# Optimization experiments

Hardware: AMD Instinct MI355X
Metric: run time of the kernel (lower is better)

Reference implementation:

```python
import jax, jax.numpy as jnp
import numpy as np
from jax import lax

N_KERNELS = 11
N_GRAMS = 3
EMB = 300
CONV_OUT = 128
B, QLEN, DLEN = 128, 30, 256


def _kernel_mus(n):
    mus = [1.0]
    bin_size = 2.0 / (n - 1)
    mus.append(1 - bin_size / 2)
    for i in range(1, n - 1):
        mus.append(mus[i] - bin_size)
    return mus


def _kernel_sigmas(n):
    bin_size = 2.0 / (n - 1)
    return [0.001] + [0.5 * bin_size] * (n - 1)


MU = jnp.asarray(np.array(_kernel_mus(N_KERNELS), dtype=np.float32))      # [K]
SIGMA = jnp.asarray(np.array(_kernel_sigmas(N_KERNELS), dtype=np.float32))  # [K]


def setup_inputs() -> dict:
    key = jax.random.key(0)
    ks = jax.random.split(key, 10)
    inp = {
        "query_embeddings": jax.random.normal(ks[0], (B, QLEN, EMB), jnp.float32),
        "document_embeddings": jax.random.normal(ks[1], (B, DLEN, EMB), jnp.float32),
        "query_pad_oov_mask": jnp.ones((B, QLEN), jnp.float32),
        "document_pad_oov_mask": jnp.ones((B, DLEN), jnp.float32),
    }
    # conv weights for n-gram sizes 1..3: [out_ch, in_ch, ksize]
    for i in range(1, N_GRAMS + 1):
        inp[f"conv_w{i}"] = jax.random.normal(ks[1 + i], (CONV_OUT, EMB, i), jnp.float32) * 0.05
        inp[f"conv_b{i}"] = jnp.zeros((CONV_OUT,), jnp.float32)
    inp["dense_w"] = jax.random.uniform(ks[9], (1, N_KERNELS * N_GRAMS * N_GRAMS), jnp.float32,
                                        minval=-0.014, maxval=0.014)
    return inp


def _conv_ngram(x, w, b):
    # x: [B, L, E]; w: [C, E, k]; right-pad by k-1 so output length == L (ConstantPad1d((0,k-1)))
    k = w.shape[-1]
    y = lax.conv_general_dilated(x.transpose(0, 2, 1), w, (1,), [(0, k - 1)],
                                 dimension_numbers=("NCH", "OIH", "NCH"))
    return jax.nn.relu(y + b[None, :, None]).transpose(0, 2, 1)  # [B, L, C]


def _kernel_pool(q, d, qd_mask, q_mask):
    # cosine matrix (AllenNLP CosineMatrixAttention: normalize with +1e-13 eps)
    qn = q / (jnp.linalg.norm(q, axis=-1, keepdims=True) + 1e-13)
    dn = d / (jnp.linalg.norm(d, axis=-1, keepdims=True) + 1e-13)
    cos = jnp.einsum("bqe,bde->bqd", qn, dn) * qd_mask  # [B, Q, D]
    # RBF soft-histogram kernels: [B, Q, D, K]
    k = jnp.exp(-(cos[..., None] - MU) ** 2 / (2.0 * SIGMA ** 2)) * qd_mask[..., None]
    per_kernel_query = k.sum(axis=2)  # [B, Q, K]
    log_pk = jnp.log(jnp.clip(per_kernel_query, 1e-10, None)) * 0.01
    return (log_pk * q_mask[..., None]).sum(axis=1)  # [B, K]


def reference(query_embeddings, document_embeddings, query_pad_oov_mask, document_pad_oov_mask,
              conv_w1, conv_b1, conv_w2, conv_b2, conv_w3, conv_b3, dense_w):
    qd_mask = query_pad_oov_mask[:, :, None] * document_pad_oov_mask[:, None, :]  # [B, Q, D]
    conv_params = [(conv_w1, conv_b1), (conv_w2, conv_b2), (conv_w3, conv_b3)]
    q_res = [_conv_ngram(query_embeddings, w, b) for w, b in conv_params]
    d_res = [_conv_ngram(document_embeddings, w, b) for w, b in conv_params]
    matched = [_kernel_pool(q_res[i], d_res[t], qd_mask, query_pad_oov_mask)
               for i in range(N_GRAMS) for t in range(N_GRAMS)]
    all_grams = jnp.concatenate(matched, axis=1)  # [B, K*9]
    return jnp.squeeze(all_grams @ dense_w.T, axis=1)  # [B]
```

## Files before the change

kernel.cpp:

```cpp
#include <hip/hip_runtime.h>
#include <math.h>


typedef __bf16 bf16x8 __attribute__((ext_vector_type(8)));
typedef float f32x4 __attribute__((ext_vector_type(4)));

#if __has_builtin(__builtin_amdgcn_exp2f)
#define EXP2F(x) __builtin_amdgcn_exp2f(x)
#else
#define EXP2F(x) exp2f(x)
#endif

#define AS_STRIDE 344

static __device__ __forceinline__ unsigned short f2bf(float f) {
  union { float f; unsigned int u; } v; v.f = f;
  unsigned int r = v.u + 0x7FFFu + ((v.u >> 16) & 1u);
  return (unsigned short)(r >> 16);
}

__global__ __launch_bounds__(256) void prep_w(
    const float* __restrict__ w1, const float* __restrict__ w2,
    const float* __restrict__ w3, unsigned short* __restrict__ wt2) {
  int idx = blockIdx.x * 256 + threadIdx.x;
  if (idx >= 245760) return;
  int jj   = idx & 7;
  int lane = (idx >> 3) & 63;
  int ec   = (idx >> 9) % 10;
  int cb   = (idx / 5120) & 7;
  int p    = idx / 40960;
  const float* w; int k, jt;
  if (p == 0)      { w = w1; k = 1; jt = 0; }
  else if (p <= 2) { w = w2; k = 2; jt = p - 1; }
  else             { w = w3; k = 3; jt = p - 3; }
  int c = cb * 16 + (lane & 15);
  int e = ec * 32 + (lane >> 4) * 8 + jj;
  float v = (e < 300) ? w[(c * 300 + e) * k + jt] : 0.0f;
  wt2[idx] = f2bf(v);
}

template<int NI>
__device__ __forceinline__ void conv_body(
    unsigned short* As, float* psq,
    const float* __restrict__ xs, int L, int l0, int b,
    const unsigned short* __restrict__ wt2,
    const float* __restrict__ b1, const float* __restrict__ b2,
    const float* __restrict__ b3,
    unsigned short* __restrict__ out) {
  constexpr int ROWS = NI * 16 + 2;
  constexpr int NR = NI * 16;
  const int t = threadIdx.x;
  const int w = __builtin_amdgcn_readfirstlane(t >> 6);
  const int lane = t & 63;
  const int quad = lane >> 4, lrow = lane & 15;

  for (int idx = t; idx < ROWS * 40; idx += 512) {
    int r = idx / 40, c = idx % 40;
    int l = l0 + r;
    int e = c * 8;
    float4 a = make_float4(0.f, 0.f, 0.f, 0.f);
    float4 cc = make_float4(0.f, 0.f, 0.f, 0.f);
    if (l < L) {
      const float* src = xs + (size_t)l * 300;
      if (e < 300)     a  = *reinterpret_cast<const float4*>(src + e);
      if (e + 4 < 300) cc = *reinterpret_cast<const float4*>(src + e + 4);
    }
    uint4 o;
    o.x = (unsigned int)f2bf(a.x) | ((unsigned int)f2bf(a.y) << 16);
    o.y = (unsigned int)f2bf(a.z) | ((unsigned int)f2bf(a.w) << 16);
    o.z = (unsigned int)f2bf(cc.x) | ((unsigned int)f2bf(cc.y) << 16);
    o.w = (unsigned int)f2bf(cc.z) | ((unsigned int)f2bf(cc.w) << 16);
    *reinterpret_cast<uint4*>(&As[r * AS_STRIDE + c * 8]) = o;
  }

  f32x4 acc[NI][3];
  #pragma unroll
  for (int ni = 0; ni < NI; ++ni)
    #pragma unroll
    for (int g = 0; g < 3; ++g) acc[ni][g] = (f32x4){0.f, 0.f, 0.f, 0.f};

  const unsigned short* wl = wt2 + (size_t)lane * 8;

  auto wfld = [&](bf16x8* dst, int ec) {
    #pragma unroll
    for (int p = 0; p < 6; ++p)
      dst[p] = *reinterpret_cast<const bf16x8*>(
          wl + ((((p * 8 + w) * 10 + ec) << 9)));
  };

  auto compute = [&](const bf16x8* wf, int ec) {
    bf16x8 xf[3][NI];
    #pragma unroll
    for (int j = 0; j < 3; ++j)
      #pragma unroll
      for (int ni = 0; ni < NI; ++ni)
        xf[j][ni] = *reinterpret_cast<const bf16x8*>(
            &As[(ni * 16 + lrow + j) * AS_STRIDE + ec * 32 + quad * 8]);
    const int PJ[6] = {0, 0, 1, 0, 1, 2};
    const int PG[6] = {0, 1, 1, 2, 2, 2};
    #pragma unroll
    for (int p = 0; p < 6; ++p)
      #pragma unroll
      for (int ni = 0; ni < NI; ++ni)
        acc[ni][PG[p]] = __builtin_amdgcn_mfma_f32_16x16x32_bf16(
            wf[p], xf[PJ[p]][ni], acc[ni][PG[p]], 0, 0, 0);
  };

  bf16x8 wfA[6], wfB[6];
  wfld(wfA, 0);
  __syncthreads();

  #pragma unroll
  for (int ec = 0; ec < 10; ec += 2) {
    wfld(wfB, ec + 1);
    compute(wfA, ec);
    if (ec + 2 < 10) wfld(wfA, ec + 2);
    compute(wfB, ec + 1);
  }

  const float* biases[3] = {b1, b2, b3};
  float4 bv[3];
  #pragma unroll
  for (int g = 0; g < 3; ++g)
    bv[g] = *reinterpret_cast<const float4*>(biases[g] + w * 16 + quad * 4);

  #pragma unroll
  for (int ni = 0; ni < NI; ++ni) {
    #pragma unroll
    for (int g = 0; g < 3; ++g) {
      float p = 0.f;
      #pragma unroll
      for (int r = 0; r < 4; ++r) {
        float y = fmaxf(acc[ni][g][r] + bv[g][r], 0.f);
        p += y * y;
      }
      p += __shfl_xor(p, 16);
      p += __shfl_xor(p, 32);
      if (lane < 16) psq[(w * 3 + g) * NR + ni * 16 + lrow] = p;
    }
  }
  __syncthreads();

  #pragma unroll
  for (int ni = 0; ni < NI; ++ni) {
    int row = ni * 16 + lrow;
    int l = l0 + row;
    if (l < L) {
      #pragma unroll
      for (int g = 0; g < 3; ++g) {
        float ssq = 0.f;
        #pragma unroll
        for (int wv = 0; wv < 8; ++wv) ssq += psq[(wv * 3 + g) * NR + row];
        float inv = 1.0f / (sqrtf(ssq) + 1e-13f);
        unsigned int pk[2];
        #pragma unroll
        for (int h = 0; h < 2; ++h) {
          float y0 = fmaxf(acc[ni][g][2 * h + 0] + bv[g][2 * h + 0], 0.f) * inv;
          float y1 = fmaxf(acc[ni][g][2 * h + 1] + bv[g][2 * h + 1], 0.f) * inv;
          pk[h] = (unsigned int)f2bf(y0) | ((unsigned int)f2bf(y1) << 16);
        }
        unsigned short* op = out + ((size_t)(g * 128 + b) * L + l) * 128 +
                             w * 16 + quad * 4;
        *reinterpret_cast<uint2*>(op) = make_uint2(pk[0], pk[1]);
      }
    }
  }
}

__global__ __launch_bounds__(512, 4) void conv_all(
    const float* __restrict__ qemb, const float* __restrict__ demb,
    const unsigned short* __restrict__ wt2,
    const float* __restrict__ b1, const float* __restrict__ b2,
    const float* __restrict__ b3,
    unsigned short* __restrict__ qn, unsigned short* __restrict__ dn) {
  __shared__ unsigned short As[34 * AS_STRIDE];
  __shared__ float psq[8 * 3 * 32];
  const int bi = blockIdx.x;
  if (bi < 1024)
    conv_body<2>(As, psq, demb + (size_t)(bi >> 3) * 256 * 300, 256,
                 (bi & 7) * 32, bi >> 3, wt2, b1, b2, b3, dn);
  else
    conv_body<2>(As, psq, qemb + (size_t)(bi - 1024) * 30 * 300, 30,
                 0, bi - 1024, wt2, b1, b2, b3, qn);
}

__global__ __launch_bounds__(64) void pool_mfma(
    const unsigned short* __restrict__ qn, const unsigned short* __restrict__ dn,
    const float* __restrict__ qmask, const float* __restrict__ dmask,
    float* __restrict__ pkq8) {
  const float A2[11] = {2.0f, 1.8f, 1.4f, 1.0f, 0.6f, 0.2f,
                        -0.2f, -0.6f, -1.0f, -1.4f, -1.8f};
  const float CC[11] = {-721347.52f, -58.429149f, -35.346028f, -18.033688f,
                        -6.4921277f, -0.72134752f, -0.72134752f, -6.4921277f,
                        -18.033688f, -35.346028f, -58.429149f};
  const int tg    = blockIdx.x >> 3;
  const int chunk = blockIdx.x & 7;
  const int b     = blockIdx.y;
  const int lane  = threadIdx.x;
  const int quad  = lane >> 4, l15 = lane & 15;
  const int d0    = chunk * 32;

  const unsigned short* dslab = dn + (size_t)(tg * 128 + b) * 256 * 128;

  bf16x8 aD[2][4];
  #pragma unroll
  for (int mi = 0; mi < 2; ++mi)
    #pragma unroll
    for (int kt = 0; kt < 4; ++kt)
      aD[mi][kt] = *reinterpret_cast<const bf16x8*>(
          dslab + (size_t)(d0 + mi * 16 + l15) * 128 + kt * 32 + quad * 8);

  float dmv[2][4];
  #pragma unroll
  for (int mi = 0; mi < 2; ++mi)
    #pragma unroll
    for (int r = 0; r < 4; ++r)
      dmv[mi][r] = dmask[b * 256 + d0 + mi * 16 + quad * 4 + r];

  float qmv[2];
  qmv[0] = qmask[b * 30 + l15];
  qmv[1] = (16 + l15 < 30) ? qmask[b * 30 + 16 + l15] : 0.0f;

  #pragma unroll 1
  for (int ig = 0; ig < 3; ++ig) {
    const unsigned short* qslab = qn + (size_t)(ig * 128 + b) * 30 * 128;

    bf16x8 bQ[2][4];
    #pragma unroll
    for (int ni = 0; ni < 2; ++ni)
      #pragma unroll
      for (int kt = 0; kt < 4; ++kt)
        bQ[ni][kt] = *reinterpret_cast<const bf16x8*>(
            qslab + (size_t)(ni * 16 + l15) * 128 + kt * 32 + quad * 8);

    f32x4 acc[2][2];
    #pragma unroll
    for (int mi = 0; mi < 2; ++mi)
      #pragma unroll
      for (int ni = 0; ni < 2; ++ni) acc[mi][ni] = (f32x4){0.f, 0.f, 0.f, 0.f};

    #pragma unroll
    for (int kt = 0; kt < 4; ++kt)
      #pragma unroll
      for (int mi = 0; mi < 2; ++mi)
        #pragma unroll
        for (int ni = 0; ni < 2; ++ni)
          acc[mi][ni] = __builtin_amdgcn_mfma_f32_16x16x32_bf16(
              aD[mi][kt], bQ[ni][kt], acc[mi][ni], 0, 0, 0);

    float feat[2][11];
    #pragma unroll
    for (int ni = 0; ni < 2; ++ni)
      #pragma unroll
      for (int kk = 0; kk < 11; ++kk) feat[ni][kk] = 0.0f;

    #pragma unroll
    for (int mi = 0; mi < 2; ++mi) {
      #pragma unroll
      for (int r = 0; r < 4; ++r) {
        #pragma unroll
        for (int ni = 0; ni < 2; ++ni) {
          float m  = qmv[ni] * dmv[mi][r];
          float cm = acc[mi][ni][r] * m;
          float w0 = cm * -721347.52f;
          float w1 = cm * -72.134752f;
          #pragma unroll
          for (int kk = 0; kk < 11; ++kk) {
            float wk = (kk == 0) ? w0 : w1;
            float e = EXP2F(fmaf(wk, cm - A2[kk], CC[kk]));
            feat[ni][kk] += e * m;
          }
        }
      }
    }

    #pragma unroll
    for (int ni = 0; ni < 2; ++ni)
      #pragma unroll
      for (int kk = 0; kk < 11; ++kk) {
        float v = feat[ni][kk];
        v += __shfl_xor(v, 16);
        v += __shfl_xor(v, 32);
        feat[ni][kk] = v;
      }

    if (quad == 0) {
      const int pair = ig * 3 + tg;
      #pragma unroll
      for (int ni = 0; ni < 2; ++ni) {
        int q = ni * 16 + l15;
        if (q < 30) {
          float* p = pkq8 +
              (((size_t)(chunk * 9 + pair) * 128 + b) * 30 + q) * 11;
          #pragma unroll
          for (int kk = 0; kk < 11; ++kk) p[kk] = feat[ni][kk];
        }
      }
    }
  }
}

__global__ __launch_bounds__(256) void final_kernel(
    const float* __restrict__ pkq8, const float* __restrict__ qmask,
    const float* __restrict__ dw, float* __restrict__ out) {
  const int CH = 9 * 128 * 30 * 11;
  const int b = blockIdx.x;
  const int t = threadIdx.x;
  float s = 0.0f;
  for (int idx = t; idx < 9 * 30 * 11; idx += 256) {
    int pair = idx / 330;
    int rem  = idx % 330;
    int q    = rem / 11;
    int kk   = rem % 11;
    size_t base = (((size_t)pair * 128 + b) * 30 + q) * 11 + kk;
    float v = 0.f;
    #pragma unroll
    for (int c = 0; c < 8; ++c) v += pkq8[base + (size_t)c * CH];
    s += __logf(fmaxf(v, 1e-10f)) * 0.01f * qmask[b * 30 + q] * dw[pair * 11 + kk];
  }
  s += __shfl_xor(s, 1);  s += __shfl_xor(s, 2);  s += __shfl_xor(s, 4);
  s += __shfl_xor(s, 8);  s += __shfl_xor(s, 16); s += __shfl_xor(s, 32);
  __shared__ float part[4];
  if ((t & 63) == 0) part[t >> 6] = s;
  __syncthreads();
  if (t == 0) out[b] = part[0] + part[1] + part[2] + part[3];
}

extern "C" void kernel_launch(void* const* d_in, const int* in_sizes, int n_in,
                              void* d_out, int out_size, void* d_ws, size_t ws_size,
                              hipStream_t stream) {
  const float* qemb  = (const float*)d_in[0];
  const float* demb  = (const float*)d_in[1];
  const float* qmask = (const float*)d_in[2];
  const float* dmask = (const float*)d_in[3];
  const float* w1 = (const float*)d_in[4];
  const float* b1 = (const float*)d_in[5];
  const float* w2 = (const float*)d_in[6];
  const float* b2 = (const float*)d_in[7];
  const float* w3 = (const float*)d_in[8];
  const float* b3 = (const float*)d_in[9];
  const float* dw = (const float*)d_in[10];

  unsigned short* ws  = (unsigned short*)d_ws;
  unsigned short* wt2 = ws;
  unsigned short* qn  = ws + 12042240;
  unsigned short* dn  = ws + 13516800;
  float*          pkq8 = (float*)(ws + 245760);
  float* out = (float*)d_out;

  prep_w<<<960, 256, 0, stream>>>(w1, w2, w3, wt2);
  conv_all<<<1152, 512, 0, stream>>>(qemb, demb, wt2, b1, b2, b3, qn, dn);
  pool_mfma<<<dim3(24, 128), 64, 0, stream>>>(qn, dn, qmask, dmask, pkq8);
  final_kernel<<<128, 256, 0, stream>>>(pkq8, qmask, dw, out);
}
```

Measured before the change: 163.9 us.

## Fuse final reduction into pool kernel via atomics and last-block completion counter

Pool blocks no longer write eight per-chunk partial histograms for a separate final kernel. They atomically accumulate into one zeroed buffer, and the last of the 24 blocks per batch (found with a per-batch atomic counter) computes the log, mask and dense dot product. The zeroing of the accumulator and counters is folded into the weight-prep launch. This removes one kernel launch and the 8x partial-buffer round trip, at the cost of float atomics, non-deterministic summation order and a threadfence-based completion protocol.

```diff
diff --git a/kernel.cpp b/kernel.cpp
--- a/kernel.cpp
+++ b/kernel.cpp
@@ -21,9 +21,16 @@
 
 __global__ __launch_bounds__(256) void prep_w(
     const float* __restrict__ w1, const float* __restrict__ w2,
-    const float* __restrict__ w3, unsigned short* __restrict__ wt2) {
-  int idx = blockIdx.x * 256 + threadIdx.x;
-  if (idx >= 245760) return;
+    const float* __restrict__ w3, unsigned short* __restrict__ wt2,
+    float* __restrict__ pkq, unsigned int* __restrict__ cnt) {
+  const int bid = blockIdx.x;
+  if (bid >= 960) {
+    int idx = (bid - 960) * 256 + threadIdx.x;
+    if (idx < 380160) pkq[idx] = 0.0f;
+    if (idx < 128) cnt[idx] = 0u;
+    return;
+  }
+  int idx = bid * 256 + threadIdx.x;
   int jj   = idx & 7;
   int lane = (idx >> 3) & 63;
   int ec   = (idx >> 9) % 10;
@@ -184,10 +191,12 @@
                  0, bi - 1024, wt2, b1, b2, b3, qn);
 }
 
-__global__ __launch_bounds__(64) void pool_mfma(
+__global__ __launch_bounds__(64) void pool_finish(
     const unsigned short* __restrict__ qn, const unsigned short* __restrict__ dn,
     const float* __restrict__ qmask, const float* __restrict__ dmask,
-    float* __restrict__ pkq8) {
+    const float* __restrict__ dw,
+    float* __restrict__ pkq, unsigned int* __restrict__ cnt,
+    float* __restrict__ out) {
   const float A2[11] = {2.0f, 1.8f, 1.4f, 1.0f, 0.6f, 0.2f,
                         -0.2f, -0.6f, -1.0f, -1.4f, -1.8f};
   const float CC[11] = {-721347.52f, -58.429149f, -35.346028f, -18.033688f,
@@ -263,10 +272,10 @@
           float m  = qmv[ni] * dmv[mi][r];
           float cm = acc[mi][ni][r] * m;
           float w0 = cm * -721347.52f;
-          float w1 = cm * -72.134752f;
+          float w1c = cm * -72.134752f;
           #pragma unroll
           for (int kk = 0; kk < 11; ++kk) {
-            float wk = (kk == 0) ? w0 : w1;
+            float wk = (kk == 0) ? w0 : w1c;
             float e = EXP2F(fmaf(wk, cm - A2[kk], CC[kk]));
             feat[ni][kk] += e * m;
           }
@@ -290,40 +299,34 @@
       for (int ni = 0; ni < 2; ++ni) {
         int q = ni * 16 + l15;
         if (q < 30) {
-          float* p = pkq8 +
-              (((size_t)(chunk * 9 + pair) * 128 + b) * 30 + q) * 11;
+          float* p = pkq + (((size_t)pair * 128 + b) * 30 + q) * 11;
           #pragma unroll
-          for (int kk = 0; kk < 11; ++kk) p[kk] = feat[ni][kk];
+          for (int kk = 0; kk < 11; ++kk) atomicAdd(p + kk, feat[ni][kk]);
         }
       }
     }
   }
-}
-
-__global__ __launch_bounds__(256) void final_kernel(
-    const float* __restrict__ pkq8, const float* __restrict__ qmask,
-    const float* __restrict__ dw, float* __restrict__ out) {
-  const int CH = 9 * 128 * 30 * 11;
-  const int b = blockIdx.x;
-  const int t = threadIdx.x;
-  float s = 0.0f;
-  for (int idx = t; idx < 9 * 30 * 11; idx += 256) {
-    int pair = idx / 330;
-    int rem  = idx % 330;
-    int q    = rem / 11;
-    int kk   = rem % 11;
-    size_t base = (((size_t)pair * 128 + b) * 30 + q) * 11 + kk;
-    float v = 0.f;
-    #pragma unroll
-    for (int c = 0; c < 8; ++c) v += pkq8[base + (size_t)c * CH];
-    s += __logf(fmaxf(v, 1e-10f)) * 0.01f * qmask[b * 30 + q] * dw[pair * 11 + kk];
-  }
-  s += __shfl_xor(s, 1);  s += __shfl_xor(s, 2);  s += __shfl_xor(s, 4);
-  s += __shfl_xor(s, 8);  s += __shfl_xor(s, 16); s += __shfl_xor(s, 32);
-  __shared__ float part[4];
-  if ((t & 63) == 0) part[t >> 6] = s;
-  __syncthreads();
-  if (t == 0) out[b] = part[0] + part[1] + part[2] + part[3];
+
+  __threadfence();
+  unsigned int prev0 = 0;
+  if (lane == 0) prev0 = atomicAdd(&cnt[b], 1u);
+  unsigned int prev = __shfl((int)prev0, 0);
+  if (prev == 23u) {
+    __threadfence();
+    float s = 0.0f;
+    for (int idx = lane; idx < 330; idx += 64) {
+      int q = idx / 11, kk = idx % 11;
+      float qm = qmask[b * 30 + q] * 0.01f;
+      #pragma unroll
+      for (int pair = 0; pair < 9; ++pair) {
+        float v = pkq[(((size_t)pair * 128 + b) * 30 + q) * 11 + kk];
+        s += __logf(fmaxf(v, 1e-10f)) * qm * dw[pair * 11 + kk];
+      }
+    }
+    s += __shfl_xor(s, 1);  s += __shfl_xor(s, 2);  s += __shfl_xor(s, 4);
+    s += __shfl_xor(s, 8);  s += __shfl_xor(s, 16); s += __shfl_xor(s, 32);
+    if (lane == 0) out[b] = s;
+  }
 }
 
 extern "C" void kernel_launch(void* const* d_in, const int* in_sizes, int n_in,
@@ -343,13 +346,14 @@
 
   unsigned short* ws  = (unsigned short*)d_ws;
   unsigned short* wt2 = ws;
+  float*          pkq = (float*)(ws + 245760);
+  unsigned int*   cnt = (unsigned int*)(pkq + 380160);
   unsigned short* qn  = ws + 12042240;
   unsigned short* dn  = ws + 13516800;
-  float*          pkq8 = (float*)(ws + 245760);
   float* out = (float*)d_out;
 
-  prep_w<<<960, 256, 0, stream>>>(w1, w2, w3, wt2);
+  prep_w<<<2445, 256, 0, stream>>>(w1, w2, w3, wt2, pkq, cnt);
   conv_all<<<1152, 512, 0, stream>>>(qemb, demb, wt2, b1, b2, b3, qn, dn);
-  pool_mfma<<<dim3(24, 128), 64, 0, stream>>>(qn, dn, qmask, dmask, pkq8);
-  final_kernel<<<128, 256, 0, stream>>>(pkq8, qmask, dw, out);
-}
+  pool_finish<<<dim3(24, 128), 64, 0, stream>>>(qn, dn, qmask, dmask, dw,
+                                                pkq, cnt, out);
+}
```

Result: slower. 313.0 us (+90.9%).
